# Optimization experiments

Measured on AMD Instinct MI355X. Metric: run time of the kernel, lower is better.

## Reference

```python
import jax, jax.numpy as jnp
import numpy as np

N = 400000
C_IN = 64
C_OUT = 64
K = 27  # 3x3x3 kernel offsets
EPS = 1e-4


def _subm_conv(feat, nbr_t, W):
    # feat: [N, Cin], nbr_t: [K, N] int32, W: [K, Cin, Cout]
    # rulebook-style gather-GEMM-scatter: accumulate over kernel offsets
    def body(acc, kw):
        Wk, idxk = kw
        return acc + feat[idxk] @ Wk, None
    init = jnp.zeros((feat.shape[0], W.shape[-1]), feat.dtype)
    out, _ = jax.lax.scan(body, init, (W, nbr_t))
    return out


def _bn(x, g, b):
    # BatchNorm1d with track_running_stats=False: always uses batch stats
    m = x.mean(axis=0)
    v = x.var(axis=0)
    return (x - m) * jax.lax.rsqrt(v + EPS) * g + b


def _lrelu(x, slope):
    return jnp.where(x >= 0, x, slope * x)


def setup_inputs() -> dict:
    key = jax.random.key(0)
    ks = jax.random.split(key, 11)
    features = jax.random.normal(ks[0], (N, C_IN), dtype=jnp.float32)
    neighbor_idx = jax.random.randint(ks[1], (N, K), 0, N, dtype=jnp.int32)
    s = 0.05
    W1 = jax.random.normal(ks[2], (K, C_IN, C_OUT), dtype=jnp.float32) * s
    W2 = jax.random.normal(ks[3], (K, C_OUT, C_OUT), dtype=jnp.float32) * s
    W3 = jax.random.normal(ks[4], (K, C_OUT, C_OUT), dtype=jnp.float32) * s
    g1 = jax.random.normal(ks[5], (C_OUT,), dtype=jnp.float32) * 0.1 + 1.0
    b1 = jax.random.normal(ks[6], (C_OUT,), dtype=jnp.float32) * 0.1
    g2 = jax.random.normal(ks[7], (C_OUT,), dtype=jnp.float32) * 0.1 + 1.0
    b2 = jax.random.normal(ks[8], (C_OUT,), dtype=jnp.float32) * 0.1
    g3 = jax.random.normal(ks[9], (C_OUT,), dtype=jnp.float32) * 0.1 + 1.0
    b3 = jax.random.normal(ks[10], (C_OUT,), dtype=jnp.float32) * 0.1
    return {"features": features, "neighbor_idx": neighbor_idx,
            "W1": W1, "g1": g1, "b1": b1,
            "W2": W2, "g2": g2, "b2": b2,
            "W3": W3, "g3": g3, "b3": b3}


def reference(features, neighbor_idx, W1, g1, b1, W2, g2, b2, W3, g3, b3):
    nbr_t = neighbor_idx.T  # [K, N]
    # conv_block1: subm conv -> BN -> LeakyReLU(0.05)
    x = _lrelu(_bn(_subm_conv(features, nbr_t, W1), g1, b1), 0.05)
    res = x
    # conv_block2
    x = _lrelu(_bn(_subm_conv(x, nbr_t, W2), g2, b2), 0.05)
    # conv_block3 (no activation) + norm
    x = _bn(_subm_conv(x, nbr_t, W3), g3, b3)
    # residual add + scn.LeakyReLU (default leakiness = 1/3)
    return _lrelu(x + res, 0.333)
```

## Files before the change

kernel.cpp:

```cpp
#include <hip/hip_runtime.h>
#include <hip/hip_bf16.h>

#define N_PTS 400000
#define KOFF 27
#define AP 72

typedef __attribute__((ext_vector_type(8))) short short8;
typedef __attribute__((ext_vector_type(4))) float float4v;

__device__ __forceinline__ unsigned short f2bf(float f) {
    union { float f; unsigned int u; } a; a.f = f;
    unsigned int u = a.u;
    unsigned int r = (u + 0x7FFFu + ((u >> 16) & 1u)) >> 16;
    return (unsigned short)r;
}

__device__ __forceinline__ float bf2f(unsigned short u) {
    union { unsigned int u; float f; } a; a.u = ((unsigned int)u) << 16;
    return a.f;
}

__global__ void prep_kernel(const float* __restrict__ feat,
                            unsigned short* __restrict__ B0,
                            const float* __restrict__ W1,
                            const float* __restrict__ W2,
                            const float* __restrict__ W3,
                            unsigned short* __restrict__ Wt,
                            float* __restrict__ stats) {
    int b = blockIdx.x;
    int tid = threadIdx.x;
    if (b < 25000) {
        int i = b * 256 + tid;
        const float4* s4 = (const float4*)feat;
        float4 v = s4[i];
        ushort4 o;
        o.x = f2bf(v.x); o.y = f2bf(v.y); o.z = f2bf(v.z); o.w = f2bf(v.w);
        ((ushort4*)B0)[i] = o;
    } else {
        int i = (b - 25000) * 256 + tid;
        if (i < 384) stats[i] = 0.0f;
        if (i >= KOFF * 64 * 64) return;
        int k = i >> 12;
        int co = (i >> 6) & 63;
        int ci = i & 63;
        int src = (k << 12) + (ci << 6) + co;
        const int WS = KOFF * 4096;
        Wt[i] = f2bf(W1[src]);
        Wt[i + WS] = f2bf(W2[src]);
        Wt[i + 2 * WS] = f2bf(W3[src]);
    }
}

template<int OUTBF>
__global__ __launch_bounds__(512, 8)
void conv_kernel(const unsigned short* __restrict__ X,
                 const int* __restrict__ nbr,
                 const unsigned short* __restrict__ Wt,
                 void* __restrict__ Yout,
                 float* __restrict__ stats) {
    __shared__ unsigned short lds_a[128 * AP];
    __shared__ unsigned short lds_w[64 * AP];
    const int tid = threadIdx.x;
    const int wave = tid >> 6;
    const int lane = tid & 63;
    const int quad = lane >> 4;
    const int l16 = lane & 15;
    const int p0 = blockIdx.x * 128;

    const int sr = tid >> 2;
    const int sq = tid & 3;
    const int wr = tid >> 3;
    const int wc = (tid & 7) << 3;

    float4v acc[4];
    #pragma unroll
    for (int t = 0; t < 4; ++t) acc[t] = (float4v){0.f, 0.f, 0.f, 0.f};

    const long nb = (long)(p0 + sr) * KOFF;
    int gi = nbr[nb];
    int gin = nbr[nb + 1];
    uint4 a0, a1, w0;
    {
        const uint4* srcA = (const uint4*)(X + ((size_t)gi << 6)) + sq * 2;
        a0 = srcA[0];
        a1 = srcA[1];
        w0 = ((const uint4*)Wt)[tid];
    }

    for (int k = 0; k < KOFF; ++k) {
        __syncthreads();
        *(uint4*)(lds_a + sr * AP + sq * 16) = a0;
        *(uint4*)(lds_a + sr * AP + sq * 16 + 8) = a1;
        *(uint4*)(lds_w + wr * AP + wc) = w0;
        if (k < KOFF - 1) {
            const uint4* srcA = (const uint4*)(X + ((size_t)gin << 6)) + sq * 2;
            a0 = srcA[0];
            a1 = srcA[1];
            w0 = ((const uint4*)(Wt + (((size_t)(k + 1)) << 12)))[tid];
            gin = (k < KOFF - 2) ? nbr[nb + k + 2] : 0;
        }
        __syncthreads();
        const int abase = (wave * 16 + l16) * AP + quad * 8;
        #pragma unroll
        for (int ks = 0; ks < 2; ++ks) {
            short8 af = *(const short8*)(lds_a + abase + ks * 32);
            #pragma unroll
            for (int t = 0; t < 4; ++t) {
                short8 bf = *(const short8*)(lds_w + (t * 16 + l16) * AP + ks * 32 + quad * 8);
                acc[t] = __builtin_amdgcn_mfma_f32_16x16x32_bf16(af, bf, acc[t], 0, 0, 0);
            }
        }
    }

    const int row_base = p0 + wave * 16 + quad * 4;
    #pragma unroll
    for (int t = 0; t < 4; ++t) {
        #pragma unroll
        for (int r = 0; r < 4; ++r) {
            size_t idx = (size_t)(row_base + r) * 64 + t * 16 + l16;
            if (OUTBF) {
                __builtin_nontemporal_store(f2bf(acc[t][r]),
                                            (unsigned short*)Yout + idx);
            } else {
                __builtin_nontemporal_store(acc[t][r], (float*)Yout + idx);
            }
        }
    }

    __syncthreads();
    float* red = (float*)lds_w;
    if (tid < 128) red[tid] = 0.0f;
    __syncthreads();
    #pragma unroll
    for (int t = 0; t < 4; ++t) {
        float s = acc[t][0] + acc[t][1] + acc[t][2] + acc[t][3];
        float ss = acc[t][0] * acc[t][0] + acc[t][1] * acc[t][1] +
                   acc[t][2] * acc[t][2] + acc[t][3] * acc[t][3];
        s += __shfl_down(s, 32);
        s += __shfl_down(s, 16);
        ss += __shfl_down(ss, 32);
        ss += __shfl_down(ss, 16);
        if (lane < 16) {
            atomicAdd(&red[t * 16 + l16], s);
            atomicAdd(&red[64 + t * 16 + l16], ss);
        }
    }
    __syncthreads();
    if (tid < 128) atomicAdd(&stats[tid], red[tid]);
}

__global__ void bnact_kernel(const unsigned short* __restrict__ Yb,
                             const float* __restrict__ stats,
                             const float* __restrict__ g, const float* __restrict__ b,
                             unsigned short* __restrict__ Xb, float slope) {
    __shared__ float scale[64], shift[64];
    int tid = threadIdx.x;
    if (tid < 64) {
        float m = stats[tid] * (1.0f / N_PTS);
        float v = stats[64 + tid] * (1.0f / N_PTS) - m * m;
        float rs = rsqrtf(v + 1e-4f);
        float sc = rs * g[tid];
        scale[tid] = sc;
        shift[tid] = b[tid] - m * sc;
    }
    __syncthreads();
    int i = blockIdx.x * blockDim.x + tid;
    const int total = N_PTS * 16;
    if (i >= total) return;
    int cb = (i & 15) << 2;
    ushort4 y4 = ((const ushort4*)Yb)[i];
    float o0 = bf2f(y4.x) * scale[cb] + shift[cb];
    float o1 = bf2f(y4.y) * scale[cb + 1] + shift[cb + 1];
    float o2 = bf2f(y4.z) * scale[cb + 2] + shift[cb + 2];
    float o3 = bf2f(y4.w) * scale[cb + 3] + shift[cb + 3];
    o0 = o0 >= 0.f ? o0 : slope * o0;
    o1 = o1 >= 0.f ? o1 : slope * o1;
    o2 = o2 >= 0.f ? o2 : slope * o2;
    o3 = o3 >= 0.f ? o3 : slope * o3;
    ushort4 o;
    o.x = f2bf(o0); o.y = f2bf(o1); o.z = f2bf(o2); o.w = f2bf(o3);
    ((ushort4*)Xb)[i] = o;
}

__global__ void bnact_final_kernel(float* __restrict__ Y, const float* __restrict__ stats,
                                   const float* __restrict__ g, const float* __restrict__ b,
                                   const unsigned short* __restrict__ res) {
    __shared__ float scale[64], shift[64];
    int tid = threadIdx.x;
    if (tid < 64) {
        float m = stats[tid] * (1.0f / N_PTS);
        float v = stats[64 + tid] * (1.0f / N_PTS) - m * m;
        float rs = rsqrtf(v + 1e-4f);
        float sc = rs * g[tid];
        scale[tid] = sc;
        shift[tid] = b[tid] - m * sc;
    }
    __syncthreads();
    int i = blockIdx.x * blockDim.x + tid;
    const int total = N_PTS * 16;
    if (i >= total) return;
    int cb = (i & 15) << 2;
    float4 y = ((const float4*)Y)[i];
    ushort4 r4 = ((const ushort4*)res)[i];
    float o0 = y.x * scale[cb] + shift[cb] + bf2f(r4.x);
    float o1 = y.y * scale[cb + 1] + shift[cb + 1] + bf2f(r4.y);
    float o2 = y.z * scale[cb + 2] + shift[cb + 2] + bf2f(r4.z);
    float o3 = y.w * scale[cb + 3] + shift[cb + 3] + bf2f(r4.w);
    o0 = o0 >= 0.f ? o0 : 0.333f * o0;
    o1 = o1 >= 0.f ? o1 : 0.333f * o1;
    o2 = o2 >= 0.f ? o2 : 0.333f * o2;
    o3 = o3 >= 0.f ? o3 : 0.333f * o3;
    float4 o; o.x = o0; o.y = o1; o.z = o2; o.w = o3;
    ((float4*)Y)[i] = o;
}

extern "C" void kernel_launch(void* const* d_in, const int* in_sizes, int n_in,
                              void* d_out, int out_size, void* d_ws, size_t ws_size,
                              hipStream_t stream) {
    const float* feat = (const float*)d_in[0];
    const int* nbr = (const int*)d_in[1];
    const float* W1 = (const float*)d_in[2];
    const float* g1 = (const float*)d_in[3];
    const float* b1 = (const float*)d_in[4];
    const float* W2 = (const float*)d_in[5];
    const float* g2 = (const float*)d_in[6];
    const float* b2 = (const float*)d_in[7];
    const float* W3 = (const float*)d_in[8];
    const float* g3 = (const float*)d_in[9];
    const float* b3 = (const float*)d_in[10];
    float* Y = (float*)d_out;
    unsigned short* Ybf = (unsigned short*)d_out;

    char* ws = (char*)d_ws;
    const size_t BF_BYTES = (size_t)N_PTS * 64 * 2;
    unsigned short* B0 = (unsigned short*)ws;
    unsigned short* B1 = (unsigned short*)(ws + BF_BYTES);
    unsigned short* Wt = (unsigned short*)(ws + 2 * BF_BYTES);
    float* stats = (float*)(ws + 2 * BF_BYTES + (size_t)3 * KOFF * 4096 * 2);

    const int WSTRIDE = KOFF * 4096;

    prep_kernel<<<25432, 256, 0, stream>>>(feat, B0, W1, W2, W3, Wt, stats);

    conv_kernel<1><<<N_PTS / 128, 512, 0, stream>>>(B0, nbr, Wt, (void*)Ybf, stats);
    bnact_kernel<<<25000, 256, 0, stream>>>(Ybf, stats, g1, b1, B1, 0.05f);
    conv_kernel<1><<<N_PTS / 128, 512, 0, stream>>>(B1, nbr, Wt + WSTRIDE, (void*)Ybf, stats + 128);
    bnact_kernel<<<25000, 256, 0, stream>>>(Ybf, stats + 128, g2, b2, B0, 0.05f);
    conv_kernel<0><<<N_PTS / 128, 512, 0, stream>>>(B0, nbr, Wt + 2 * WSTRIDE, (void*)Y, stats + 256);
    bnact_final_kernel<<<25000, 256, 0, stream>>>(Y, stats + 256, g3, b3, B1);
}
```

Baseline: 1.016 ms.

## Fuse BatchNorm+LeakyReLU into next conv's gather and stage bf16 output through LDS

Result: slower. 1.437 ms (+41.4%).

```diff
diff --git a/kernel.cpp b/kernel.cpp
--- a/kernel.cpp
+++ b/kernel.cpp
@@ -7,6 +7,7 @@
 
 typedef __attribute__((ext_vector_type(8))) short short8;
 typedef __attribute__((ext_vector_type(4))) float float4v;
+typedef __attribute__((ext_vector_type(4))) unsigned int uint4v;
 
 __device__ __forceinline__ unsigned short f2bf(float f) {
     union { float f; unsigned int u; } a; a.f = f;
@@ -51,15 +52,31 @@
     }
 }
 
-template<int OUTBF>
+__device__ __forceinline__ uint4 bn_u4(uint4 q, const float* S, const float* B, int c0) {
+    union { uint4 q; unsigned short s[8]; } u;
+    u.q = q;
+    #pragma unroll
+    for (int j = 0; j < 8; ++j) {
+        float f = bf2f(u.s[j]) * S[c0 + j] + B[c0 + j];
+        f = f >= 0.f ? f : 0.05f * f;
+        u.s[j] = f2bf(f);
+    }
+    return u.q;
+}
+
+template<int OUTBF, int APPLY_BN>
 __global__ __launch_bounds__(512, 8)
 void conv_kernel(const unsigned short* __restrict__ X,
                  const int* __restrict__ nbr,
                  const unsigned short* __restrict__ Wt,
                  void* __restrict__ Yout,
-                 float* __restrict__ stats) {
+                 float* __restrict__ stats,
+                 const float* __restrict__ pstats,
+                 const float* __restrict__ pg,
+                 const float* __restrict__ pb) {
     __shared__ unsigned short lds_a[128 * AP];
     __shared__ unsigned short lds_w[64 * AP];
+    __shared__ float bnS[64], bnB[64];
     const int tid = threadIdx.x;
     const int wave = tid >> 6;
     const int lane = tid & 63;
@@ -71,6 +88,15 @@
     const int sq = tid & 3;
     const int wr = tid >> 3;
     const int wc = (tid & 7) << 3;
+
+    if (APPLY_BN && tid < 64) {
+        float m = pstats[tid] * (1.0f / N_PTS);
+        float v = pstats[64 + tid] * (1.0f / N_PTS) - m * m;
+        float rs = rsqrtf(v + 1e-4f);
+        float sc = rs * pg[tid];
+        bnS[tid] = sc;
+        bnB[tid] = pb[tid] - m * sc;
+    }
 
     float4v acc[4];
     #pragma unroll
@@ -89,8 +115,13 @@
 
     for (int k = 0; k < KOFF; ++k) {
         __syncthreads();
-        *(uint4*)(lds_a + sr * AP + sq * 16) = a0;
-        *(uint4*)(lds_a + sr * AP + sq * 16 + 8) = a1;
+        if (APPLY_BN) {
+            *(uint4*)(lds_a + sr * AP + sq * 16) = bn_u4(a0, bnS, bnB, sq * 16);
+            *(uint4*)(lds_a + sr * AP + sq * 16 + 8) = bn_u4(a1, bnS, bnB, sq * 16 + 8);
+        } else {
+            *(uint4*)(lds_a + sr * AP + sq * 16) = a0;
+            *(uint4*)(lds_a + sr * AP + sq * 16 + 8) = a1;
+        }
         *(uint4*)(lds_w + wr * AP + wc) = w0;
         if (k < KOFF - 1) {
             const uint4* srcA = (const uint4*)(X + ((size_t)gin << 6)) + sq * 2;
@@ -112,25 +143,40 @@
         }
     }
 
-    const int row_base = p0 + wave * 16 + quad * 4;
-    #pragma unroll
-    for (int t = 0; t < 4; ++t) {
+    float* red = (float*)lds_w;
+    if (OUTBF) {
+        __syncthreads();
+        {
+            const int rl = wave * 16 + quad * 4;
+            #pragma unroll
+            for (int t = 0; t < 4; ++t)
+                #pragma unroll
+                for (int r = 0; r < 4; ++r)
+                    lds_a[(rl + r) * 64 + t * 16 + l16] = f2bf(acc[t][r]);
+        }
+        if (tid < 128) red[tid] = 0.0f;
+        __syncthreads();
+        {
+            const uint4v* lc = (const uint4v*)lds_a;
+            uint4v* dst = (uint4v*)((unsigned short*)Yout + (size_t)p0 * 64);
+            __builtin_nontemporal_store(lc[tid * 2], dst + tid * 2);
+            __builtin_nontemporal_store(lc[tid * 2 + 1], dst + tid * 2 + 1);
+        }
+    } else {
+        const int row_base = p0 + wave * 16 + quad * 4;
         #pragma unroll
-        for (int r = 0; r < 4; ++r) {
-            size_t idx = (size_t)(row_base + r) * 64 + t * 16 + l16;
-            if (OUTBF) {
-                __builtin_nontemporal_store(f2bf(acc[t][r]),
-                                            (unsigned short*)Yout + idx);
-            } else {
+        for (int t = 0; t < 4; ++t) {
+            #pragma unroll
+            for (int r = 0; r < 4; ++r) {
+                size_t idx = (size_t)(row_base + r) * 64 + t * 16 + l16;
                 __builtin_nontemporal_store(acc[t][r], (float*)Yout + idx);
             }
         }
-    }
-
-    __syncthreads();
-    float* red = (float*)lds_w;
-    if (tid < 128) red[tid] = 0.0f;
-    __syncthreads();
+        __syncthreads();
+        if (tid < 128) red[tid] = 0.0f;
+        __syncthreads();
+    }
+
     #pragma unroll
     for (int t = 0; t < 4; ++t) {
         float s = acc[t][0] + acc[t][1] + acc[t][2] + acc[t][3];
@@ -149,51 +195,27 @@
     if (tid < 128) atomicAdd(&stats[tid], red[tid]);
 }
 
-__global__ void bnact_kernel(const unsigned short* __restrict__ Yb,
-                             const float* __restrict__ stats,
-                             const float* __restrict__ g, const float* __restrict__ b,
-                             unsigned short* __restrict__ Xb, float slope) {
-    __shared__ float scale[64], shift[64];
+__global__ void bnact_final_kernel(float* __restrict__ Y,
+                                   const float* __restrict__ stats3,
+                                   const float* __restrict__ g3, const float* __restrict__ b3,
+                                   const unsigned short* __restrict__ Y1raw,
+                                   const float* __restrict__ stats1,
+                                   const float* __restrict__ g1, const float* __restrict__ b1) {
+    __shared__ float sc3[64], sh3[64], sc1[64], sh1[64];
     int tid = threadIdx.x;
     if (tid < 64) {
-        float m = stats[tid] * (1.0f / N_PTS);
-        float v = stats[64 + tid] * (1.0f / N_PTS) - m * m;
+        float m = stats3[tid] * (1.0f / N_PTS);
+        float v = stats3[64 + tid] * (1.0f / N_PTS) - m * m;
         float rs = rsqrtf(v + 1e-4f);
-        float sc = rs * g[tid];
-        scale[tid] = sc;
-        shift[tid] = b[tid] - m * sc;
-    }
-    __syncthreads();
-    int i = blockIdx.x * blockDim.x + tid;
-    const int total = N_PTS * 16;
-    if (i >= total) return;
-    int cb = (i & 15) << 2;
-    ushort4 y4 = ((const ushort4*)Yb)[i];
-    float o0 = bf2f(y4.x) * scale[cb] + shift[cb];
-    float o1 = bf2f(y4.y) * scale[cb + 1] + shift[cb + 1];
-    float o2 = bf2f(y4.z) * scale[cb + 2] + shift[cb + 2];
-    float o3 = bf2f(y4.w) * scale[cb + 3] + shift[cb + 3];
-    o0 = o0 >= 0.f ? o0 : slope * o0;
-    o1 = o1 >= 0.f ? o1 : slope * o1;
-    o2 = o2 >= 0.f ? o2 : slope * o2;
-    o3 = o3 >= 0.f ? o3 : slope * o3;
-    ushort4 o;
-    o.x = f2bf(o0); o.y = f2bf(o1); o.z = f2bf(o2); o.w = f2bf(o3);
-    ((ushort4*)Xb)[i] = o;
-}
-
-__global__ void bnact_final_kernel(float* __restrict__ Y, const float* __restrict__ stats,
-                                   const float* __restrict__ g, const float* __restrict__ b,
-                                   const unsigned short* __restrict__ res) {
-    __shared__ float scale[64], shift[64];
-    int tid = threadIdx.x;
-    if (tid < 64) {
-        float m = stats[tid] * (1.0f / N_PTS);
-        float v = stats[64 + tid] * (1.0f / N_PTS) - m * m;
-        float rs = rsqrtf(v + 1e-4f);
-        float sc = rs * g[tid];
-        scale[tid] = sc;
-        shift[tid] = b[tid] - m * sc;
+        float sc = rs * g3[tid];
+        sc3[tid] = sc;
+        sh3[tid] = b3[tid] - m * sc;
+        m = stats1[tid] * (1.0f / N_PTS);
+        v = stats1[64 + tid] * (1.0f / N_PTS) - m * m;
+        rs = rsqrtf(v + 1e-4f);
+        sc = rs * g1[tid];
+        sc1[tid] = sc;
+        sh1[tid] = b1[tid] - m * sc;
     }
     __syncthreads();
     int i = blockIdx.x * blockDim.x + tid;
@@ -201,11 +223,19 @@
     if (i >= total) return;
     int cb = (i & 15) << 2;
     float4 y = ((const float4*)Y)[i];
-    ushort4 r4 = ((const ushort4*)res)[i];
-    float o0 = y.x * scale[cb] + shift[cb] + bf2f(r4.x);
-    float o1 = y.y * scale[cb + 1] + shift[cb + 1] + bf2f(r4.y);
-    float o2 = y.z * scale[cb + 2] + shift[cb + 2] + bf2f(r4.z);
-    float o3 = y.w * scale[cb + 3] + shift[cb + 3] + bf2f(r4.w);
+    ushort4 r4 = ((const ushort4*)Y1raw)[i];
+    float r0 = bf2f(r4.x) * sc1[cb] + sh1[cb];
+    float r1 = bf2f(r4.y) * sc1[cb + 1] + sh1[cb + 1];
+    float r2 = bf2f(r4.z) * sc1[cb + 2] + sh1[cb + 2];
+    float r3 = bf2f(r4.w) * sc1[cb + 3] + sh1[cb + 3];
+    r0 = r0 >= 0.f ? r0 : 0.05f * r0;
+    r1 = r1 >= 0.f ? r1 : 0.05f * r1;
+    r2 = r2 >= 0.f ? r2 : 0.05f * r2;
+    r3 = r3 >= 0.f ? r3 : 0.05f * r3;
+    float o0 = y.x * sc3[cb] + sh3[cb] + r0;
+    float o1 = y.y * sc3[cb + 1] + sh3[cb + 1] + r1;
+    float o2 = y.z * sc3[cb + 2] + sh3[cb + 2] + r2;
+    float o3 = y.w * sc3[cb + 3] + sh3[cb + 3] + r3;
     o0 = o0 >= 0.f ? o0 : 0.333f * o0;
     o1 = o1 >= 0.f ? o1 : 0.333f * o1;
     o2 = o2 >= 0.f ? o2 : 0.333f * o2;
@@ -229,7 +259,6 @@
     const float* g3 = (const float*)d_in[9];
     const float* b3 = (const float*)d_in[10];
     float* Y = (float*)d_out;
-    unsigned short* Ybf = (unsigned short*)d_out;
 
     char* ws = (char*)d_ws;
     const size_t BF_BYTES = (size_t)N_PTS * 64 * 2;
@@ -242,10 +271,12 @@
 
     prep_kernel<<<25432, 256, 0, stream>>>(feat, B0, W1, W2, W3, Wt, stats);
 
-    conv_kernel<1><<<N_PTS / 128, 512, 0, stream>>>(B0, nbr, Wt, (void*)Ybf, stats);
-    bnact_kernel<<<25000, 256, 0, stream>>>(Ybf, stats, g1, b1, B1, 0.05f);
-    conv_kernel<1><<<N_PTS / 128, 512, 0, stream>>>(B1, nbr, Wt + WSTRIDE, (void*)Ybf, stats + 128);
-    bnact_kernel<<<25000, 256, 0, stream>>>(Ybf, stats + 128, g2, b2, B0, 0.05f);
-    conv_kernel<0><<<N_PTS / 128, 512, 0, stream>>>(B0, nbr, Wt + 2 * WSTRIDE, (void*)Y, stats + 256);
-    bnact_final_kernel<<<25000, 256, 0, stream>>>(Y, stats + 256, g3, b3, B1);
-}
+    conv_kernel<1, 0><<<N_PTS / 128, 512, 0, stream>>>(
+        B0, nbr, Wt, (void*)B1, stats, stats, g1, b1);
+    conv_kernel<1, 1><<<N_PTS / 128, 512, 0, stream>>>(
+        B1, nbr, Wt + WSTRIDE, (void*)B0, stats + 128, stats, g1, b1);
+    conv_kernel<0, 1><<<N_PTS / 128, 512, 0, stream>>>(
+        B0, nbr, Wt + 2 * WSTRIDE, (void*)Y, stats + 256, stats + 128, g2, b2);
+    bnact_final_kernel<<<25000, 256, 0, stream>>>(
+        Y, stats + 256, g3, b3, B1, stats, g1, b1);
+}
```
